# Performance work log

Hardware: AMD Instinct MI355X
Metric: run time of the kernel (lower is better)

Reference implementation:

```python
import jax, jax.numpy as jnp
import numpy as np

NEG_SLOPE = 0.2
EPS = 1e-16  # PyG softmax denominator epsilon


def gat_conv(x, src, dst, W, att_src, att_dst, bias, concat):
    """One PyG-style GATConv layer (eval mode, self-loops already in src/dst).
    x: [N, F_in]; src/dst: [E]; W: [F_in, H*C]; att_*: [H, C]; bias: [H*C] or [C].
    """
    N = x.shape[0]
    H, C = att_src.shape
    h = (x @ W).reshape(N, H, C)                        # [N,H,C]
    a_s = jnp.sum(h * att_src[None], axis=-1)           # [N,H]
    a_d = jnp.sum(h * att_dst[None], axis=-1)           # [N,H]
    alpha = jax.nn.leaky_relu(a_s[src] + a_d[dst], NEG_SLOPE)  # [E,H]
    # segment softmax over incoming edges of each destination node
    m = jax.ops.segment_max(alpha, dst, num_segments=N)        # [N,H]
    alpha = jnp.exp(alpha - m[dst])
    denom = jax.ops.segment_sum(alpha, dst, num_segments=N)    # [N,H]
    alpha = alpha / (denom[dst] + EPS)
    # attention dropout is identity in eval mode
    out = jax.ops.segment_sum(h[src] * alpha[:, :, None], dst, num_segments=N)  # [N,H,C]
    out = out.reshape(N, H * C) if concat else out.mean(axis=1)
    return out + bias


def setup_inputs() -> dict:
    key = jax.random.key(0)
    ks = jax.random.split(key, 10)
    N, E, F_in, H, C1, F_out = 100000, 1600000, 128, 4, 32, 64
    hid = H * C1
    x = jax.random.normal(ks[0], (N, F_in), dtype=jnp.float32)
    edge_index = jax.random.randint(ks[1], (2, E), 0, N, dtype=jnp.int64)
    s = 1.0 / np.sqrt(F_in)
    W1 = jax.random.uniform(ks[2], (F_in, hid), minval=-s, maxval=s, dtype=jnp.float32)
    att_src1 = jax.random.normal(ks[3], (H, C1), dtype=jnp.float32) * 0.1
    att_dst1 = jax.random.normal(ks[4], (H, C1), dtype=jnp.float32) * 0.1
    b1 = jnp.zeros((hid,), dtype=jnp.float32)
    s2 = 1.0 / np.sqrt(hid)
    W2 = jax.random.uniform(ks[5], (hid, F_out), minval=-s2, maxval=s2, dtype=jnp.float32)
    att_src2 = jax.random.normal(ks[6], (1, F_out), dtype=jnp.float32) * 0.1
    att_dst2 = jax.random.normal(ks[7], (1, F_out), dtype=jnp.float32) * 0.1
    b2 = jnp.zeros((F_out,), dtype=jnp.float32)
    return {"x": x, "edge_index": edge_index,
            "W1": W1, "att_src1": att_src1, "att_dst1": att_dst1, "b1": b1,
            "W2": W2, "att_src2": att_src2, "att_dst2": att_dst2, "b2": b2}


def reference(x, edge_index, W1, att_src1, att_dst1, b1, W2, att_src2, att_dst2, b2):
    N = x.shape[0]
    loops = jnp.arange(N, dtype=edge_index.dtype)
    src = jnp.concatenate([edge_index[0], loops])  # add_self_loops=True (PyG default)
    dst = jnp.concatenate([edge_index[1], loops])
    h = gat_conv(x, src, dst, W1, att_src1, att_dst1, b1, concat=True)
    h = jax.nn.relu(h)  # dropout is identity in eval mode
    return gat_conv(h, src, dst, W2, att_src2, att_dst2, b2, concat=False)
```

## Files before the change

kernel.cpp:

```cpp
#include <hip/hip_runtime.h>
#include <hip/hip_bf16.h>

#define DEV static __device__ __forceinline__

typedef __attribute__((ext_vector_type(4))) float f32x4;
typedef __attribute__((ext_vector_type(8))) short bf16x8;
typedef __attribute__((ext_vector_type(8))) _Float16 half8;
typedef __attribute__((ext_vector_type(2))) _Float16 half2v;
typedef __attribute__((ext_vector_type(8))) unsigned short u16x8;

#define ESTRIDE 10240

DEV float leakys(float v) { return v > 0.f ? v : 0.2f * v; }
DEV float4 add4(float4 a, float4 b) { return make_float4(a.x+b.x, a.y+b.y, a.z+b.z, a.w+b.w); }
DEV float4 leaky4(float4 v) { return make_float4(leakys(v.x), leakys(v.y), leakys(v.z), leakys(v.w)); }
DEV float4 exp4(float4 v) { return make_float4(__expf(v.x), __expf(v.y), __expf(v.z), __expf(v.w)); }
DEV float pick4(float4 v, int i) {
    float r = v.x;
    r = (i == 1) ? v.y : r;
    r = (i == 2) ? v.z : r;
    r = (i == 3) ? v.w : r;
    return r;
}

DEV ushort f2bf(float f) {
    union { float f; unsigned u; } v; v.f = f;
    unsigned u = v.u;
    unsigned r = (u + 0x7FFFu + ((u >> 16) & 1u)) >> 16;
    return (ushort)r;
}
DEV float bf2f(ushort h) {
    union { unsigned u; float f; } v; v.u = ((unsigned)h) << 16;
    return v.f;
}
DEV ushort f2h(float f) {
    union { _Float16 h; ushort u; } v;
    v.h = (_Float16)f;
    return v.u;
}
DEV half2v u2h2(ushort2 u) {
    union { ushort2 u; half2v h; } v; v.u = u;
    return v.h;
}

__global__ void prep_w(const float* __restrict__ W, ushort* __restrict__ Wth,
                       ushort* __restrict__ Wtl, int NC) {
    int i = blockIdx.x * 256 + threadIdx.x;
    if (i >= 128 * NC) return;
    int k = i / NC, n = i % NC;
    float v = W[i];
    ushort hi = f2bf(v);
    ushort lo = f2bf(v - bf2f(hi));
    Wth[n * 128 + k] = hi;
    Wtl[n * 128 + k] = lo;
}

template <int NCOLS, bool AH>
__launch_bounds__(256, 2)
__global__ void gemm_mfma(const float* __restrict__ A, const ushort* __restrict__ A16,
                          const ushort* __restrict__ Wth, const ushort* __restrict__ Wtl,
                          ushort* __restrict__ C16,
                          const float* __restrict__ att_s, const float* __restrict__ att_d,
                          float* __restrict__ as_out, float* __restrict__ ad_out, int N,
                          const int* __restrict__ srcIdx, const int* __restrict__ dstIdx,
                          int* __restrict__ bcursor, uint2* __restrict__ ebuf,
                          int E, int nGemmBlocks) {
    constexpr int NT = NCOLS / 64;
    __shared__ ushort Xhi[64 * 128];
    __shared__ ushort Xlo[64 * 128];
    __shared__ float pbs[64][4];
    __shared__ float pbd[64][4];
    const int t = threadIdx.x;

    if (blockIdx.x >= nGemmBlocks) {
        __shared__ int hist[256];
        __shared__ int gofs[256];
        hist[t] = 0;
        __syncthreads();
        int blk = blockIdx.x - nGemmBlocks;
        int e0 = blk * 4096;
        int e1 = min(E, e0 + 4096);
        for (int e = e0 + t; e < e1; e += 256)
            atomicAdd(&hist[dstIdx[e] >> 9], 1);
        __syncthreads();
        int h = hist[t];
        if (h) gofs[t] = atomicAdd(&bcursor[t], h);
        __syncthreads();
        hist[t] = 0;
        __syncthreads();
        for (int e = e0 + t; e < e1; e += 256) {
            int d = dstIdx[e];
            int b = d >> 9;
            int r = atomicAdd(&hist[b], 1);
            uint2 v; v.x = (unsigned)srcIdx[e]; v.y = (unsigned)d;
            ebuf[(size_t)b * ESTRIDE + gofs[b] + r] = v;
        }
        return;
    }

    const int wv = t >> 6, l = t & 63;
    const int l15 = l & 15, lhi = l >> 4;
    const int row0 = blockIdx.x * 64;
    const int n0 = wv * 16 * NT;

    if constexpr (!AH) {
        for (int i = t; i < 2048; i += 256) {
            int r = i >> 5, c4 = i & 31;
            int gr = row0 + r;
            float4 v = make_float4(0.f, 0.f, 0.f, 0.f);
            if (gr < N) v = ((const float4*)A)[(size_t)gr * 32 + c4];
            ushort4 hi, lo;
            hi.x = f2bf(v.x); lo.x = f2bf(v.x - bf2f(hi.x));
            hi.y = f2bf(v.y); lo.y = f2bf(v.y - bf2f(hi.y));
            hi.z = f2bf(v.z); lo.z = f2bf(v.z - bf2f(hi.z));
            hi.w = f2bf(v.w); lo.w = f2bf(v.w - bf2f(hi.w));
            int idx = (r * 128 + c4 * 4) ^ ((r & 7) << 3);
            *(ushort4*)&Xhi[idx] = hi;
            *(ushort4*)&Xlo[idx] = lo;
        }
    } else {
        for (int i = t; i < 1024; i += 256) {
            int r = i >> 4, c8 = i & 15;
            int gr = row0 + r;
            half8 v = (half8){0, 0, 0, 0, 0, 0, 0, 0};
            if (gr < N) v = *(const half8*)&A16[(size_t)gr * 128 + c8 * 8];
            u16x8 hi, lo;
#pragma unroll
            for (int j = 0; j < 8; j++) {
                float f = (float)v[j];
                ushort hb = f2bf(f);
                hi[j] = hb;
                lo[j] = f2bf(f - bf2f(hb));
            }
            int idx = (r * 128 + c8 * 8) ^ ((r & 7) << 3);
            *(u16x8*)&Xhi[idx] = hi;
            *(u16x8*)&Xlo[idx] = lo;
        }
    }
    __syncthreads();

    f32x4 acc[4][NT];
#pragma unroll
    for (int mt = 0; mt < 4; mt++)
#pragma unroll
        for (int nt = 0; nt < NT; nt++) acc[mt][nt] = (f32x4){0.f, 0.f, 0.f, 0.f};

#pragma unroll
    for (int ks = 0; ks < 4; ks++) {
        bf16x8 ah[4], al[4];
#pragma unroll
        for (int mt = 0; mt < 4; mt++) {
            int row = mt * 16 + l15;
            int idx = (row * 128 + ks * 32 + lhi * 8) ^ ((row & 7) << 3);
            ah[mt] = *(const bf16x8*)&Xhi[idx];
            al[mt] = *(const bf16x8*)&Xlo[idx];
        }
#pragma unroll
        for (int nt = 0; nt < NT; nt++) {
            size_t wo = (size_t)(n0 + nt * 16 + l15) * 128 + ks * 32 + lhi * 8;
            bf16x8 bh = *(const bf16x8*)&Wth[wo];
            bf16x8 bl = *(const bf16x8*)&Wtl[wo];
#pragma unroll
            for (int mt = 0; mt < 4; mt++) {
                acc[mt][nt] = __builtin_amdgcn_mfma_f32_16x16x32_bf16(ah[mt], bh, acc[mt][nt], 0, 0, 0);
                acc[mt][nt] = __builtin_amdgcn_mfma_f32_16x16x32_bf16(ah[mt], bl, acc[mt][nt], 0, 0, 0);
                acc[mt][nt] = __builtin_amdgcn_mfma_f32_16x16x32_bf16(al[mt], bh, acc[mt][nt], 0, 0, 0);
            }
        }
    }
#pragma unroll
    for (int mt = 0; mt < 4; mt++) {
#pragma unroll
        for (int j = 0; j < 4; j++) {
            int gr = row0 + mt * 16 + lhi * 4 + j;
            if (gr < N) {
#pragma unroll
                for (int nt = 0; nt < NT; nt++)
                    C16[(size_t)gr * NCOLS + n0 + nt * 16 + l15] = f2h(acc[mt][nt][j]);
            }
        }
    }
    if constexpr (NT == 2) {
        float as0 = att_s[n0 + l15],       ad0 = att_d[n0 + l15];
        float as1v = att_s[n0 + 16 + l15], ad1v = att_d[n0 + 16 + l15];
#pragma unroll
        for (int mt = 0; mt < 4; mt++) {
#pragma unroll
            for (int j = 0; j < 4; j++) {
                float ps = acc[mt][0][j] * as0 + acc[mt][1][j] * as1v;
                float pd = acc[mt][0][j] * ad0 + acc[mt][1][j] * ad1v;
#pragma unroll
                for (int o = 1; o < 16; o <<= 1) {
                    ps += __shfl_xor(ps, o);
                    pd += __shfl_xor(pd, o);
                }
                if (l15 == 0) {
                    int gr = row0 + mt * 16 + lhi * 4 + j;
                    if (gr < N) {
                        as_out[gr * 4 + wv] = ps;
                        ad_out[gr * 4 + wv] = pd;
                    }
                }
            }
        }
    } else {
        float as0 = att_s[n0 + l15], ad0 = att_d[n0 + l15];
#pragma unroll
        for (int mt = 0; mt < 4; mt++) {
#pragma unroll
            for (int j = 0; j < 4; j++) {
                float ps = acc[mt][0][j] * as0;
                float pd = acc[mt][0][j] * ad0;
#pragma unroll
                for (int o = 1; o < 16; o <<= 1) {
                    ps += __shfl_xor(ps, o);
                    pd += __shfl_xor(pd, o);
                }
                if (l15 == 0) {
                    int rl = mt * 16 + lhi * 4 + j;
                    pbs[rl][wv] = ps;
                    pbd[rl][wv] = pd;
                }
            }
        }
        __syncthreads();
        if (t < 64) {
            int gr = row0 + t;
            if (gr < N) {
                as_out[gr] = pbs[t][0] + pbs[t][1] + pbs[t][2] + pbs[t][3];
                ad_out[gr] = pbd[t][0] + pbd[t][1] + pbd[t][2] + pbd[t][3];
            }
        }
    }
}

__global__ void bfill(const uint2* __restrict__ ebuf, const int* __restrict__ bcnt,
                      int* __restrict__ rowptr, int* __restrict__ esrc,
                      int N, int NB, int E) {
    __shared__ int cnt[512];
    __shared__ int lds[256];
    __shared__ int ebase;
    int b = blockIdx.x, t = threadIdx.x;
    int n0 = b << 9;
    cnt[t] = 0; cnt[t + 256] = 0;
    int v = (t < NB) ? bcnt[t] : 0;
    lds[t] = v;
    __syncthreads();
    int val = v;
    for (int o = 1; o < 256; o <<= 1) {
        int other = (t >= o) ? lds[t - o] : 0;
        __syncthreads();
        val += other; lds[t] = val;
        __syncthreads();
    }
    if (t == b) ebase = val - v;
    __syncthreads();
    int e0 = ebase;
    int mycnt = bcnt[b];
    const uint2* eb = ebuf + (size_t)b * ESTRIDE;
    for (int i = t; i < mycnt; i += 256)
        atomicAdd(&cnt[eb[i].y & 511], 1);
    __syncthreads();
    int c0 = cnt[2 * t], c1 = cnt[2 * t + 1];
    int s = c0 + c1;
    lds[t] = s;
    __syncthreads();
    int val2 = s;
    for (int o = 1; o < 256; o <<= 1) {
        int other = (t >= o) ? lds[t - o] : 0;
        __syncthreads();
        val2 += other; lds[t] = val2;
        __syncthreads();
    }
    int p = val2 - s;
    int nrem = N - n0;
    if (2 * t < nrem)     rowptr[n0 + 2 * t]     = e0 + p;
    if (2 * t + 1 < nrem) rowptr[n0 + 2 * t + 1] = e0 + p + c0;
    cnt[2 * t] = p; cnt[2 * t + 1] = p + c0;
    __syncthreads();
    for (int i = t; i < mycnt; i += 256) {
        uint2 ed = eb[i];
        int r = atomicAdd(&cnt[ed.y & 511], 1);
        esrc[e0 + r] = (int)ed.x;
    }
    if (b == 0 && t == 0) rowptr[N] = E;
}

__launch_bounds__(256)
__global__ void aggregate1(const ushort* __restrict__ h16,
                           const float* __restrict__ as1, const float* __restrict__ ad1,
                           const int* __restrict__ rowptr, const int* __restrict__ esrc,
                           const float* __restrict__ b1, ushort* __restrict__ out1h, int N) {
    __shared__ ushort wbuf[4][4 * 40];
    __shared__ int    sbuf[4][32];
    int wid = threadIdx.x >> 6, lane = threadIdx.x & 63;
    int node = blockIdx.x * 4 + wid;
    if (node >= N) return;
    float4 asn = *(const float4*)&as1[node * 4];
    float4 adn = *(const float4*)&ad1[node * 4];
    float4 selfw = exp4(leaky4(add4(asn, adn)));
    int start = rowptr[node], end = rowptr[node + 1];

    int eidx = lane & 15, hd = lane >> 4;
    float adh1 = pick4(adn, hd);
    int q = lane >> 4, c = lane & 15;
    int hh = c >> 2;
    float esum = 0.f;
    float acc[8] = {0.f, 0.f, 0.f, 0.f, 0.f, 0.f, 0.f, 0.f};

    for (int base = start; base < end; base += 32) {
        int cnt = end - base; if (cnt > 32) cnt = 32;
        int e1i = eidx, e2i = eidx + 16;
        int s1 = 0, s2 = 0; float w1 = 0.f, w2 = 0.f;
        if (e1i < cnt) s1 = esrc[base + e1i];
        if (e2i < cnt) s2 = esrc[base + e2i];
        if (e1i < cnt) w1 = __expf(leakys(as1[s1 * 4 + hd] + adh1));
        if (e2i < cnt) w2 = __expf(leakys(as1[s2 * 4 + hd] + adh1));
        esum += w1 + w2;
        wbuf[wid][hd * 40 + e1i] = f2h(w1);
        wbuf[wid][hd * 40 + e2i] = f2h(w2);
        if (hd == 0) { sbuf[wid][e1i] = s1; sbuf[wid][e2i] = s2; }
#pragma unroll 4
        for (int i = 0; i < cnt; i += 8) {
            int i1 = i + 2 * q;
            int2 ss = *(const int2*)&sbuf[wid][i1];
            half2v wp = u2h2(*(const ushort2*)&wbuf[wid][hh * 40 + i1]);
            half8 hv1 = *(const half8*)&h16[(size_t)ss.x * 128 + c * 8];
            half8 hv2 = *(const half8*)&h16[(size_t)ss.y * 128 + c * 8];
#pragma unroll
            for (int j = 0; j < 8; j++) {
                half2v hp = {hv1[j], hv2[j]};
                acc[j] = __builtin_amdgcn_fdot2(hp, wp, acc[j], false);
            }
        }
    }
#pragma unroll
    for (int o = 1; o < 16; o <<= 1) esum += __shfl_xor(esum, o);
    float denom = __shfl(esum, hh << 4) + pick4(selfw, hh) + 1e-16f;
    float inv = 1.f / denom;
    float sw = pick4(selfw, hh);

#pragma unroll
    for (int j = 0; j < 8; j++) {
        acc[j] += __shfl_xor(acc[j], 16);
        acc[j] += __shfl_xor(acc[j], 32);
    }
    if (q == 0) {
        half8 hs = *(const half8*)&h16[(size_t)node * 128 + c * 8];
        const float* bb = &b1[c * 8];
        half8 ov;
#pragma unroll
        for (int j = 0; j < 8; j++) {
            float oj = fmaxf((acc[j] + sw * (float)hs[j]) * inv + bb[j], 0.f);
            ov[j] = (_Float16)oj;
        }
        *(half8*)&out1h[(size_t)node * 128 + c * 8] = ov;
    }
}

__launch_bounds__(256)
__global__ void aggregate2(const ushort* __restrict__ h16,
                           const float* __restrict__ as2, const float* __restrict__ ad2,
                           const int* __restrict__ rowptr, const int* __restrict__ esrc,
                           const float* __restrict__ b2, float* __restrict__ out, int N) {
    __shared__ ushort wbuf[4][64];
    __shared__ int    sbuf[4][64];
    int wid = threadIdx.x >> 6, lane = threadIdx.x & 63;
    int node = blockIdx.x * 4 + wid;
    if (node >= N) return;
    float adn = ad2[node];
    float selfw = __expf(leakys(as2[node] + adn));
    int start = rowptr[node], end = rowptr[node + 1];

    int q = lane >> 3, c = lane & 7;
    float ssum = 0.f;
    float acc[8] = {0.f, 0.f, 0.f, 0.f, 0.f, 0.f, 0.f, 0.f};

    for (int base = start; base < end; base += 64) {
        int cnt = end - base; if (cnt > 64) cnt = 64;
        int s = 0; float w = 0.f;
        if (lane < cnt) {
            s = esrc[base + lane];
            w = __expf(leakys(as2[s] + adn));
        }
        ssum += w;
        wbuf[wid][lane] = f2h(w);
        sbuf[wid][lane] = s;
#pragma unroll 4
        for (int i = 0; i < cnt; i += 16) {
            int i1 = i + 2 * q;
            int2 ss = *(const int2*)&sbuf[wid][i1];
            half2v wp = u2h2(*(const ushort2*)&wbuf[wid][i1]);
            half8 hv1 = *(const half8*)&h16[(size_t)ss.x * 64 + c * 8];
            half8 hv2 = *(const half8*)&h16[(size_t)ss.y * 64 + c * 8];
#pragma unroll
            for (int j = 0; j < 8; j++) {
                half2v hp = {hv1[j], hv2[j]};
                acc[j] = __builtin_amdgcn_fdot2(hp, wp, acc[j], false);
            }
        }
    }
#pragma unroll
    for (int o = 1; o < 64; o <<= 1) ssum += __shfl_xor(ssum, o);
    float inv = 1.f / (ssum + selfw + 1e-16f);

#pragma unroll
    for (int j = 0; j < 8; j++) {
        acc[j] += __shfl_xor(acc[j], 8);
        acc[j] += __shfl_xor(acc[j], 16);
        acc[j] += __shfl_xor(acc[j], 32);
    }
    if (lane < 8) {
        half8 hs = *(const half8*)&h16[(size_t)node * 64 + c * 8];
        const float* bb = &b2[c * 8];
        float o[8];
#pragma unroll
        for (int j = 0; j < 8; j++)
            o[j] = (acc[j] + selfw * (float)hs[j]) * inv + bb[j];
        float4* op = (float4*)&out[(size_t)node * 64 + c * 8];
        op[0] = make_float4(o[0], o[1], o[2], o[3]);
        op[1] = make_float4(o[4], o[5], o[6], o[7]);
    }
}

extern "C" void kernel_launch(void* const* d_in, const int* in_sizes, int n_in,
                              void* d_out, int out_size, void* d_ws, size_t ws_size,
                              hipStream_t stream) {
    const float* x      = (const float*)d_in[0];
    const int*   ei     = (const int*)d_in[1];
    const float* W1     = (const float*)d_in[2];
    const float* att_s1 = (const float*)d_in[3];
    const float* att_d1 = (const float*)d_in[4];
    const float* b1     = (const float*)d_in[5];
    const float* W2     = (const float*)d_in[6];
    const float* att_s2 = (const float*)d_in[7];
    const float* att_d2 = (const float*)d_in[8];
    const float* b2     = (const float*)d_in[9];

    const int N = in_sizes[0] / 128;
    const int E = in_sizes[1] / 2;
    const int NB = (N + 511) >> 9;

    char* ws = (char*)d_ws;
    size_t off = 0;
    auto alloc = [&](size_t bytes) -> void* {
        off = (off + 255) & ~(size_t)255;
        void* p = ws + off;
        off += bytes;
        return p;
    };
    ushort* h16   = (ushort*)alloc((size_t)N * 128 * 2);
    ushort* out1h = (ushort*)alloc((size_t)N * 128 * 2);
    float* as1    = (float*)alloc((size_t)N * 4 * 4);
    float* ad1    = (float*)alloc((size_t)N * 4 * 4);
    float* as2    = (float*)alloc((size_t)N * 4);
    float* ad2    = (float*)alloc((size_t)N * 4);
    int*   rowptr = (int*)alloc((size_t)(N + 1) * 4);
    int*   esrc   = (int*)alloc((size_t)E * 4);
    int*   bcursor = (int*)alloc(256 * 4);
    ushort* Wt1h  = (ushort*)alloc(128 * 128 * 2);
    ushort* Wt1l  = (ushort*)alloc(128 * 128 * 2);
    ushort* Wt2h  = (ushort*)alloc(64 * 128 * 2);
    ushort* Wt2l  = (ushort*)alloc(64 * 128 * 2);
    ushort* h16b = h16;
    uint2* ebuf = (uint2*)out1h;

    const int* srcIdx = ei;
    const int* dstIdx = ei + E;

    hipMemsetAsync(bcursor, 0, 256 * 4, stream);

    prep_w<<<64, 256, 0, stream>>>(W1, Wt1h, Wt1l, 128);
    prep_w<<<32, 256, 0, stream>>>(W2, Wt2h, Wt2l, 64);

    const int nGemm1 = (N + 63) / 64;
    const int nScat  = (E + 4095) / 4096;
    gemm_mfma<128, false><<<nGemm1 + nScat, 256, 0, stream>>>(
        x, nullptr, Wt1h, Wt1l, h16, att_s1, att_d1, as1, ad1, N,
        srcIdx, dstIdx, bcursor, ebuf, E, nGemm1);

    bfill<<<NB, 256, 0, stream>>>(ebuf, bcursor, rowptr, esrc, N, NB, E);

    aggregate1<<<(N + 3) / 4, 256, 0, stream>>>(h16, as1, ad1, rowptr, esrc,
                                                b1, out1h, N);

    const int nGemm2 = (N + 63) / 64;
    gemm_mfma<64, true><<<nGemm2, 256, 0, stream>>>(
        nullptr, out1h, Wt2h, Wt2l, h16b, att_s2, att_d2, as2, ad2, N,
        nullptr, nullptr, nullptr, nullptr, 0, nGemm2);

    aggregate2<<<(N + 3) / 4, 256, 0, stream>>>(h16b, as2, ad2, rowptr, esrc,
                                                b2, (float*)d_out, N);
}
```

Before: 222.4 us.

## Fuse layer-2 linear transform and attention logits into aggregate1 epilogue

The second GEMM kernel is removed. Each wave in aggregate1 now multiplies its freshly aggregated fp16 row by a transposed fp16 W2 held in LDS using fdot2, then writes h16b and the as2/ad2 attention logits directly. This avoids writing and re-reading the intermediate out1h buffer and saves a kernel launch. In exchange, every aggregate1 block loads about 16KB of W2 into LDS, which may lower occupancy. The GEMM also drops from split-bf16 MFMA to fp16 dot products, so precision changes.

```diff
diff --git a/kernel.cpp b/kernel.cpp
--- a/kernel.cpp
+++ b/kernel.cpp
@@ -53,6 +53,13 @@
     ushort lo = f2bf(v - bf2f(hi));
     Wth[n * 128 + k] = hi;
     Wtl[n * 128 + k] = lo;
+}
+
+__global__ void prep_w2h(const float* __restrict__ W2, ushort* __restrict__ W2t) {
+    int i = blockIdx.x * 256 + threadIdx.x;
+    if (i >= 64 * 128) return;
+    int c = i >> 7, k = i & 127;
+    W2t[c * 130 + k] = f2h(W2[k * 64 + c]);
 }
 
 template <int NCOLS, bool AH>
@@ -68,8 +75,6 @@
     constexpr int NT = NCOLS / 64;
     __shared__ ushort Xhi[64 * 128];
     __shared__ ushort Xlo[64 * 128];
-    __shared__ float pbs[64][4];
-    __shared__ float pbd[64][4];
     const int t = threadIdx.x;
 
     if (blockIdx.x >= nGemmBlocks) {
@@ -118,24 +123,6 @@
             *(ushort4*)&Xhi[idx] = hi;
             *(ushort4*)&Xlo[idx] = lo;
         }
-    } else {
-        for (int i = t; i < 1024; i += 256) {
-            int r = i >> 4, c8 = i & 15;
-            int gr = row0 + r;
-            half8 v = (half8){0, 0, 0, 0, 0, 0, 0, 0};
-            if (gr < N) v = *(const half8*)&A16[(size_t)gr * 128 + c8 * 8];
-            u16x8 hi, lo;
-#pragma unroll
-            for (int j = 0; j < 8; j++) {
-                float f = (float)v[j];
-                ushort hb = f2bf(f);
-                hi[j] = hb;
-                lo[j] = f2bf(f - bf2f(hb));
-            }
-            int idx = (r * 128 + c8 * 8) ^ ((r & 7) << 3);
-            *(u16x8*)&Xhi[idx] = hi;
-            *(u16x8*)&Xlo[idx] = lo;
-        }
     }
     __syncthreads();
 
@@ -203,34 +190,6 @@
                 }
             }
         }
-    } else {
-        float as0 = att_s[n0 + l15], ad0 = att_d[n0 + l15];
-#pragma unroll
-        for (int mt = 0; mt < 4; mt++) {
-#pragma unroll
-            for (int j = 0; j < 4; j++) {
-                float ps = acc[mt][0][j] * as0;
-                float pd = acc[mt][0][j] * ad0;
-#pragma unroll
-                for (int o = 1; o < 16; o <<= 1) {
-                    ps += __shfl_xor(ps, o);
-                    pd += __shfl_xor(pd, o);
-                }
-                if (l15 == 0) {
-                    int rl = mt * 16 + lhi * 4 + j;
-                    pbs[rl][wv] = ps;
-                    pbd[rl][wv] = pd;
-                }
-            }
-        }
-        __syncthreads();
-        if (t < 64) {
-            int gr = row0 + t;
-            if (gr < N) {
-                as_out[gr] = pbs[t][0] + pbs[t][1] + pbs[t][2] + pbs[t][3];
-                ad_out[gr] = pbd[t][0] + pbd[t][1] + pbd[t][2] + pbd[t][3];
-            }
-        }
     }
 }
 
@@ -290,14 +249,24 @@
 __global__ void aggregate1(const ushort* __restrict__ h16,
                            const float* __restrict__ as1, const float* __restrict__ ad1,
                            const int* __restrict__ rowptr, const int* __restrict__ esrc,
-                           const float* __restrict__ b1, ushort* __restrict__ out1h, int N) {
+                           const float* __restrict__ b1,
+                           const ushort* __restrict__ W2t,
+                           const float* __restrict__ att_s2, const float* __restrict__ att_d2,
+                           ushort* __restrict__ h16b, float* __restrict__ as2,
+                           float* __restrict__ ad2, int N) {
+    __shared__ ushort W2lds[64 * 130];
+    __shared__ ushort rowbuf[4][128];
     __shared__ ushort wbuf[4][4 * 40];
     __shared__ int    sbuf[4][32];
     int wid = threadIdx.x >> 6, lane = threadIdx.x & 63;
+    for (int i = threadIdx.x; i < 64 * 130; i += 256) W2lds[i] = W2t[i];
+    __syncthreads();
+
     int node = blockIdx.x * 4 + wid;
     if (node >= N) return;
     float4 asn = *(const float4*)&as1[node * 4];
     float4 adn = *(const float4*)&ad1[node * 4];
+    float atts2v = att_s2[lane], attd2v = att_d2[lane];
     float4 selfw = exp4(leaky4(add4(asn, adn)));
     int start = rowptr[node], end = rowptr[node + 1];
 
@@ -354,7 +323,24 @@
             float oj = fmaxf((acc[j] + sw * (float)hs[j]) * inv + bb[j], 0.f);
             ov[j] = (_Float16)oj;
         }
-        *(half8*)&out1h[(size_t)node * 128 + c * 8] = ov;
+        *(half8*)&rowbuf[wid][c * 8] = ov;
+    }
+    {
+        const half2v* rp = (const half2v*)&rowbuf[wid][0];
+        const half2v* wp = (const half2v*)&W2lds[lane * 130];
+        float o2 = 0.f;
+#pragma unroll
+        for (int k2 = 0; k2 < 64; k2++)
+            o2 = __builtin_amdgcn_fdot2(rp[k2], wp[k2], o2, false);
+        h16b[(size_t)node * 64 + lane] = f2h(o2);
+        float ps = o2 * atts2v;
+        float pd = o2 * attd2v;
+#pragma unroll
+        for (int o = 1; o < 64; o <<= 1) {
+            ps += __shfl_xor(ps, o);
+            pd += __shfl_xor(pd, o);
+        }
+        if (lane == 0) { as2[node] = ps; ad2[node] = pd; }
     }
 }
 
@@ -450,7 +436,8 @@
         return p;
     };
     ushort* h16   = (ushort*)alloc((size_t)N * 128 * 2);
-    ushort* out1h = (ushort*)alloc((size_t)N * 128 * 2);
+    ushort* h16b  = (ushort*)alloc((size_t)N * 64 * 2);
+    uint2*  ebuf  = (uint2*)alloc((size_t)256 * ESTRIDE * 8);
     float* as1    = (float*)alloc((size_t)N * 4 * 4);
     float* ad1    = (float*)alloc((size_t)N * 4 * 4);
     float* as2    = (float*)alloc((size_t)N * 4);
@@ -460,10 +447,7 @@
     int*   bcursor = (int*)alloc(256 * 4);
     ushort* Wt1h  = (ushort*)alloc(128 * 128 * 2);
     ushort* Wt1l  = (ushort*)alloc(128 * 128 * 2);
-    ushort* Wt2h  = (ushort*)alloc(64 * 128 * 2);
-    ushort* Wt2l  = (ushort*)alloc(64 * 128 * 2);
-    ushort* h16b = h16;
-    uint2* ebuf = (uint2*)out1h;
+    ushort* W2t   = (ushort*)alloc(64 * 130 * 2);
 
     const int* srcIdx = ei;
     const int* dstIdx = ei + E;
@@ -471,7 +455,7 @@
     hipMemsetAsync(bcursor, 0, 256 * 4, stream);
 
     prep_w<<<64, 256, 0, stream>>>(W1, Wt1h, Wt1l, 128);
-    prep_w<<<32, 256, 0, stream>>>(W2, Wt2h, Wt2l, 64);
+    prep_w2h<<<32, 256, 0, stream>>>(W2, W2t);
 
     const int nGemm1 = (N + 63) / 64;
     const int nScat  = (E + 4095) / 4096;
@@ -481,13 +465,9 @@
 
     bfill<<<NB, 256, 0, stream>>>(ebuf, bcursor, rowptr, esrc, N, NB, E);
 
-    aggregate1<<<(N + 3) / 4, 256, 0, stream>>>(h16, as1, ad1, rowptr, esrc,
-                                                b1, out1h, N);
-
-    const int nGemm2 = (N + 63) / 64;
-    gemm_mfma<64, true><<<nGemm2, 256, 0, stream>>>(
-        nullptr, out1h, Wt2h, Wt2l, h16b, att_s2, att_d2, as2, ad2, N,
-        nullptr, nullptr, nullptr, nullptr, 0, nGemm2);
+    aggregate1<<<(N + 3) / 4, 256, 0, stream>>>(h16, as1, ad1, rowptr, esrc, b1,
+                                                W2t, att_s2, att_d2,
+                                                h16b, as2, ad2, N);
 
     aggregate2<<<(N + 3) / 4, 256, 0, stream>>>(h16b, as2, ad2, rowptr, esrc,
                                                 b2, (float*)d_out, N);
```

Measured after the change: 240.3 us. 8.0% more time.
